# Performance work log

Hardware: AMD Instinct MI355X
Metric: run time of the kernel (lower is better)

The kernel has to match this reference:

```python
import jax, jax.numpy as jnp
import numpy as np

B, S, D, H = 2, 2048, 2048, 16
HD = D // H  # 128


def setup_inputs() -> dict:
    key = jax.random.key(0)
    ks = jax.random.split(key, 6)
    hidden_states = jax.random.normal(ks[0], (B, S, D), dtype=jnp.float32)
    # RoPE frequencies (llama-style): theta_j = 10000^(-2j/HD), angle = pos * theta
    inv_freq = 1.0 / (10000.0 ** (jnp.arange(0, HD, 2, dtype=jnp.float32) / HD))  # [HD/2]
    angles = jnp.arange(S, dtype=jnp.float32)[:, None] * inv_freq[None, :]  # [S, HD/2]
    freq_cos = jnp.cos(angles)
    freq_sin = jnp.sin(angles)
    # additive causal mask [1,1,S,S]
    neg = jnp.finfo(jnp.float32).min
    attention_mask = jnp.where(jnp.tril(jnp.ones((S, S), dtype=bool)), 0.0, neg)[None, None]
    std = 1.0 / np.sqrt(D)
    wq = jax.random.normal(ks[1], (D, D), dtype=jnp.float32) * std
    wk = jax.random.normal(ks[2], (D, D), dtype=jnp.float32) * std
    wv = jax.random.normal(ks[3], (D, D), dtype=jnp.float32) * std
    wo = jax.random.normal(ks[4], (D, D), dtype=jnp.float32) * std
    return dict(hidden_states=hidden_states, freq_cos=freq_cos, freq_sin=freq_sin,
                attention_mask=attention_mask, wq=wq, wk=wk, wv=wv, wo=wo)


def _apply_rope(x, cos, sin):
    # x: [B,S,H,HD]; cos/sin: [S,HD/2] broadcast to [1,S,1,HD/2]
    xr = x[..., ::2]
    xi = x[..., 1::2]
    c = cos[None, :, None, :]
    s = sin[None, :, None, :]
    or_ = xr * c - xi * s
    oi_ = xr * s + xi * c
    return jnp.stack((or_, oi_), axis=-1).reshape(x.shape)


def reference(hidden_states, freq_cos, freq_sin, attention_mask, wq, wk, wv, wo):
    bsz, q_len, _ = hidden_states.shape
    q = hidden_states @ wq.T
    k = hidden_states @ wk.T
    v = hidden_states @ wv.T
    q = q.reshape(bsz, q_len, H, HD)
    k = k.reshape(bsz, q_len, H, HD)
    v = v.reshape(bsz, q_len, H, HD)
    q = _apply_rope(q, freq_cos, freq_sin)
    k = _apply_rope(k, freq_cos, freq_sin)
    # [B,H,S,HD]
    q = q.transpose(0, 2, 1, 3)
    k = k.transpose(0, 2, 1, 3)
    v = v.transpose(0, 2, 1, 3)
    scores = jnp.einsum('bhqd,bhkd->bhqk', q, k) / jnp.sqrt(jnp.float32(HD))
    scores = scores + attention_mask
    attn = jax.nn.softmax(scores, axis=-1)
    out = jnp.einsum('bhqk,bhkd->bhqd', attn, v)
    out = out.transpose(0, 2, 1, 3).reshape(bsz, q_len, D)
    return out @ wo.T
```

## Files before the change

### kernel.cpp

```cpp
#include <hip/hip_runtime.h>

typedef unsigned short u16;
typedef unsigned int u32;
typedef __bf16 bf16x8 __attribute__((ext_vector_type(8)));
typedef float f32x4 __attribute__((ext_vector_type(4)));

#define B_ 2
#define S_ 2048
#define D_ 2048
#define H_ 16
#define HD_ 128

__device__ __forceinline__ u16 f2bf(float f) {
  u32 u = __float_as_uint(f);
  u32 r = (u + 0x7fffu + ((u >> 16) & 1u)) >> 16;
  return (u16)r;
}
__device__ __forceinline__ float bf2f(u16 b) {
  return __uint_as_float(((u32)b) << 16);
}

__device__ __forceinline__ void gll16(const void* g, void* lds) {
  __builtin_amdgcn_global_load_lds(
      (const __attribute__((address_space(1))) u32*)g,
      (__attribute__((address_space(3))) u32*)lds, 16, 0, 0);
}

__global__ __launch_bounds__(256) void cvt_bf16(const float* __restrict__ in,
                                                u16* __restrict__ out, int n4) {
  int i = blockIdx.x * 256 + threadIdx.x;
  if (i >= n4) return;
  float4 v = ((const float4*)in)[i];
  u16 o[4] __attribute__((aligned(8)));
  o[0] = f2bf(v.x); o[1] = f2bf(v.y); o[2] = f2bf(v.z); o[3] = f2bf(v.w);
  ((ushort4*)out)[i] = *(const ushort4*)o;
}

__global__ __launch_bounds__(256) void rope_k(u16* __restrict__ x,
                                              const float* __restrict__ cosb,
                                              const float* __restrict__ sinb,
                                              float scale) {
  int tid = blockIdx.x * 256 + threadIdx.x;
  int flat = tid << 3;
  int hd0 = flat & (HD_ - 1);
  int s = (flat >> 7) & (S_ - 1);
  u16 e[8] __attribute__((aligned(16)));
  *(uint4*)e = *(const uint4*)&x[flat];
  const float* cp = cosb + s * (HD_ / 2) + (hd0 >> 1);
  const float* sp = sinb + s * (HD_ / 2) + (hd0 >> 1);
#pragma unroll
  for (int i = 0; i < 4; ++i) {
    float xr = bf2f(e[2 * i]), xi = bf2f(e[2 * i + 1]);
    float c = cp[i], sn = sp[i];
    e[2 * i]     = f2bf((xr * c - xi * sn) * scale);
    e[2 * i + 1] = f2bf((xr * sn + xi * c) * scale);
  }
  *(uint4*)&x[flat] = *(const uint4*)e;
}

__global__ __launch_bounds__(256) void transpose_v(const u16* __restrict__ v,
                                                   u16* __restrict__ vt) {
  __shared__ u16 tile[64][72];
  int s0 = blockIdx.x * 64, hd0 = blockIdx.y * 64, bh = blockIdx.z;
  const u16* vh = v + (size_t)bh * S_ * HD_;
  u16* vth = vt + (size_t)bh * S_ * HD_;
  int t = threadIdx.x;
#pragma unroll
  for (int it = 0; it < 2; ++it) {
    int f = it * 256 + t;
    int r = f >> 3, c = (f & 7) * 8;
    *(uint4*)&tile[r][c] = *(const uint4*)&vh[(size_t)(s0 + r) * HD_ + hd0 + c];
  }
  __syncthreads();
#pragma unroll
  for (int it = 0; it < 2; ++it) {
    int f = it * 256 + t;
    int r = f >> 3, c = (f & 7) * 8;
    u16 tmp[8] __attribute__((aligned(16)));
#pragma unroll
    for (int j = 0; j < 8; ++j) tmp[j] = tile[c + j][r];
    *(uint4*)&vth[(size_t)(hd0 + r) * S_ + s0 + c] = *(const uint4*)tmp;
  }
}

__global__ __launch_bounds__(256) void gemm_bt(
    const u16* __restrict__ A,
    const u16* __restrict__ Wq, const u16* __restrict__ Wk, const u16* __restrict__ Wv,
    u16* __restrict__ Dq, u16* __restrict__ Dk, u16* __restrict__ Dv,
    float* __restrict__ DF, int outf32) {
  const u16* W = (blockIdx.z == 0) ? Wq : (blockIdx.z == 1) ? Wk : Wv;
  u16* Db = (blockIdx.z == 0) ? Dq : (blockIdx.z == 1) ? Dk : Dv;
  __shared__ u16 At[128 * 64] __attribute__((aligned(16)));
  __shared__ u16 Bt[128 * 64] __attribute__((aligned(16)));
  const int t = threadIdx.x, l = t & 63;
  const int w = t >> 6, wr = w >> 1, wc = w & 1;
  const int m0 = blockIdx.y * 128, n0 = blockIdx.x * 128;
  f32x4 acc[4][4];
#pragma unroll
  for (int i = 0; i < 4; ++i)
#pragma unroll
    for (int j = 0; j < 4; ++j) acc[i][j] = (f32x4){0.f, 0.f, 0.f, 0.f};
  const int row_s = t >> 3;
  const int col_s = (t & 7) * 8;
  for (int kt = 0; kt < 2048; kt += 64) {
    __syncthreads();
#pragma unroll
    for (int it = 0; it < 4; ++it) {
      int f = it * 256 + t;
      int row = it * 32 + row_s;
      gll16(&A[(size_t)(m0 + row) * 2048 + kt + col_s], &At[f * 8]);
      gll16(&W[(size_t)(n0 + row) * 2048 + kt + col_s], &Bt[f * 8]);
    }
    __syncthreads();
#pragma unroll
    for (int kk = 0; kk < 2; ++kk) {
      const int ko = kk * 32 + (l >> 4) * 8;
      bf16x8 av[4], bv[4];
#pragma unroll
      for (int i = 0; i < 4; ++i)
        av[i] = *(const bf16x8*)&At[(wr * 64 + i * 16 + (l & 15)) * 64 + ko];
#pragma unroll
      for (int i = 0; i < 4; ++i)
        bv[i] = *(const bf16x8*)&Bt[(wc * 64 + i * 16 + (l & 15)) * 64 + ko];
#pragma unroll
      for (int i = 0; i < 4; ++i)
#pragma unroll
        for (int j = 0; j < 4; ++j)
          acc[i][j] = __builtin_amdgcn_mfma_f32_16x16x32_bf16(av[i], bv[j], acc[i][j], 0, 0, 0);
    }
  }
#pragma unroll
  for (int i = 0; i < 4; ++i) {
#pragma unroll
    for (int j = 0; j < 4; ++j) {
#pragma unroll
      for (int r = 0; r < 4; ++r) {
        int m = m0 + wr * 64 + i * 16 + (l >> 4) * 4 + r;
        int n = n0 + wc * 64 + j * 16 + (l & 15);
        float val = acc[i][j][r];
        if (outf32) {
          DF[(size_t)m * 2048 + n] = val;
        } else {
          int b = m >> 11, s = m & 2047, h = n >> 7, hd = n & 127;
          Db[(((size_t)(b * 16 + h)) * 2048 + s) * 128 + hd] = f2bf(val);
        }
      }
    }
  }
}

__global__ __launch_bounds__(512) void attn_fwd(
    const u16* __restrict__ q, const u16* __restrict__ k, const u16* __restrict__ vt,
    u16* __restrict__ o) {
  const int fid = (int)blockIdx.x + 8 * (int)blockIdx.y;
  const int bh = fid & 31, xt = fid >> 5;
  const u16* qh = q + (size_t)bh * S_ * HD_;
  const u16* kh = k + (size_t)bh * S_ * HD_;
  const u16* vth = vt + (size_t)bh * S_ * HD_;
  const int t = threadIdx.x, l = t & 63, w = t >> 6;
  __shared__ u16 Kl[64][136] __attribute__((aligned(16)));
  __shared__ u16 Vl[128][72] __attribute__((aligned(16)));
  __shared__ u16 Pl[8][16][72] __attribute__((aligned(16)));
  const int b = bh >> 4, h = bh & 15;
  const int krr = t >> 4, krc = (t & 15) * 8;
  const int vrr = t >> 3, vrc = (t & 7) * 8;

  for (int half = 0; half < 2; ++half) {
    const int qb = half ? (15 - xt) : xt;
    const int q0 = qb * 128;
    const int wrow0 = q0 + w * 16;
    const int qrow = wrow0 + (l & 15);
    bf16x8 qf[4];
#pragma unroll
    for (int kk = 0; kk < 4; ++kk)
      qf[kk] = *(const bf16x8*)&qh[(size_t)qrow * HD_ + kk * 32 + (l >> 4) * 8];
    f32x4 oacc[8];
#pragma unroll
    for (int i = 0; i < 8; ++i) oacc[i] = (f32x4){0.f, 0.f, 0.f, 0.f};
    float mrow[4] = {-1e30f, -1e30f, -1e30f, -1e30f};
    float lrow[4] = {0.f, 0.f, 0.f, 0.f};

    const int ntile = 2 * qb + 2;
    for (int tk = 0; tk < ntile; ++tk) {
      const int kv0 = tk * 64;
      __syncthreads();
#pragma unroll
      for (int it = 0; it < 2; ++it) {
        int row = it * 32 + krr;
        *(uint4*)&Kl[row][krc] = *(const uint4*)&kh[(size_t)(kv0 + row) * HD_ + krc];
      }
#pragma unroll
      for (int it = 0; it < 2; ++it) {
        int row = it * 64 + vrr;
        *(uint4*)&Vl[row][vrc] = *(const uint4*)&vth[(size_t)row * S_ + kv0 + vrc];
      }
      __syncthreads();

      if (kv0 > wrow0 + 15) continue;

      f32x4 sf[4];
#pragma unroll
      for (int cb = 0; cb < 4; ++cb) sf[cb] = (f32x4){0.f, 0.f, 0.f, 0.f};
      __builtin_amdgcn_s_setprio(1);
#pragma unroll
      for (int kk = 0; kk < 4; ++kk) {
        const int ko = kk * 32 + (l >> 4) * 8;
#pragma unroll
        for (int cb = 0; cb < 4; ++cb) {
          bf16x8 bfr = *(const bf16x8*)&Kl[cb * 16 + (l & 15)][ko];
          sf[cb] = __builtin_amdgcn_mfma_f32_16x16x32_bf16(qf[kk], bfr, sf[cb], 0, 0, 0);
        }
      }
      __builtin_amdgcn_s_setprio(0);
      if (kv0 + 63 > wrow0) {
#pragma unroll
        for (int cb = 0; cb < 4; ++cb) {
          int c_abs = kv0 + cb * 16 + (l & 15);
#pragma unroll
          for (int r = 0; r < 4; ++r)
            if (c_abs > wrow0 + (l >> 4) * 4 + r) sf[cb][r] = -1e30f;
        }
      }
      float fr[4], ps[4];
#pragma unroll
      for (int r = 0; r < 4; ++r) {
        float v0 = fmaxf(fmaxf(sf[0][r], sf[1][r]), fmaxf(sf[2][r], sf[3][r]));
        v0 = fmaxf(v0, __shfl_xor(v0, 1));
        v0 = fmaxf(v0, __shfl_xor(v0, 2));
        v0 = fmaxf(v0, __shfl_xor(v0, 4));
        v0 = fmaxf(v0, __shfl_xor(v0, 8));
        float Mn = fmaxf(mrow[r], v0);
        fr[r] = exp2f(mrow[r] - Mn);
        mrow[r] = Mn;
        ps[r] = 0.f;
      }
#pragma unroll
      for (int cb = 0; cb < 4; ++cb) {
#pragma unroll
        for (int r = 0; r < 4; ++r) {
          float p = exp2f(sf[cb][r] - mrow[r]);
          ps[r] += p;
          Pl[w][(l >> 4) * 4 + r][cb * 16 + (l & 15)] = f2bf(p);
        }
      }
#pragma unroll
      for (int r = 0; r < 4; ++r) lrow[r] = lrow[r] * fr[r] + ps[r];
#pragma unroll
      for (int i = 0; i < 8; ++i)
#pragma unroll
        for (int r = 0; r < 4; ++r) oacc[i][r] *= fr[r];
      __builtin_amdgcn_s_setprio(1);
#pragma unroll
      for (int ks = 0; ks < 2; ++ks) {
        bf16x8 pa = *(const bf16x8*)&Pl[w][l & 15][ks * 32 + (l >> 4) * 8];
#pragma unroll
        for (int nf = 0; nf < 8; ++nf) {
          bf16x8 vb = *(const bf16x8*)&Vl[nf * 16 + (l & 15)][ks * 32 + (l >> 4) * 8];
          oacc[nf] = __builtin_amdgcn_mfma_f32_16x16x32_bf16(pa, vb, oacc[nf], 0, 0, 0);
        }
      }
      __builtin_amdgcn_s_setprio(0);
    }

    float inv[4];
#pragma unroll
    for (int r = 0; r < 4; ++r) {
      float s = lrow[r];
      s += __shfl_xor(s, 1);
      s += __shfl_xor(s, 2);
      s += __shfl_xor(s, 4);
      s += __shfl_xor(s, 8);
      inv[r] = 1.f / s;
    }
#pragma unroll
    for (int nf = 0; nf < 8; ++nf) {
#pragma unroll
      for (int r = 0; r < 4; ++r) {
        int row = wrow0 + (l >> 4) * 4 + r;
        int col = h * 128 + nf * 16 + (l & 15);
        o[((size_t)(b * 2048 + row)) * 2048 + col] = f2bf(oacc[nf][r] * inv[r]);
      }
    }
  }
}

extern "C" void kernel_launch(void* const* d_in, const int* in_sizes, int n_in,
                              void* d_out, int out_size, void* d_ws, size_t ws_size,
                              hipStream_t stream) {
  (void)in_sizes; (void)n_in; (void)out_size; (void)ws_size;
  const float* hs   = (const float*)d_in[0];
  const float* fcos = (const float*)d_in[1];
  const float* fsin = (const float*)d_in[2];
  const float* wq = (const float*)d_in[4];
  const float* wk = (const float*)d_in[5];
  const float* wv = (const float*)d_in[6];
  const float* wo = (const float*)d_in[7];
  float* out = (float*)d_out;
  char* ws = (char*)d_ws;
  u16* hsb = (u16*)(ws + 0);
  u16* wqb = (u16*)(ws + 16777216);
  u16* wkb = (u16*)(ws + 25165824);
  u16* wvb = (u16*)(ws + 33554432);
  u16* wob = (u16*)(ws + 41943040);
  u16* qb  = (u16*)(ws + 50331648);
  u16* kb  = (u16*)(ws + 67108864);
  u16* vb  = (u16*)(ws + 83886080);
  u16* vtb = (u16*)(ws + 100663296);
  u16* aob = (u16*)(ws + 117440512);

  cvt_bf16<<<8192, 256, 0, stream>>>(hs, hsb, 2097152);
  cvt_bf16<<<4096, 256, 0, stream>>>(wq, wqb, 1048576);
  cvt_bf16<<<4096, 256, 0, stream>>>(wk, wkb, 1048576);
  cvt_bf16<<<4096, 256, 0, stream>>>(wv, wvb, 1048576);
  cvt_bf16<<<4096, 256, 0, stream>>>(wo, wob, 1048576);

  gemm_bt<<<dim3(16, 32, 3), 256, 0, stream>>>(hsb, wqb, wkb, wvb, qb, kb, vb, nullptr, 0);

  const float qscale = (float)(0.08838834764831845 * 1.4426950408889634);
  rope_k<<<4096, 256, 0, stream>>>(qb, fcos, fsin, qscale);
  rope_k<<<4096, 256, 0, stream>>>(kb, fcos, fsin, 1.0f);

  transpose_v<<<dim3(32, 2, 32), 256, 0, stream>>>(vb, vtb);

  attn_fwd<<<dim3(8, 32), 512, 0, stream>>>(qb, kb, vtb, aob);

  gemm_bt<<<dim3(16, 32, 1), 256, 0, stream>>>(aob, wob, wob, wob,
                                               nullptr, nullptr, nullptr, out, 1);
}
```

Before: 467.0 us.

## Replace GEMM with 256x256 double-buffered swizzled-LDS pipelined kernel

Replaces the 128x128 single-buffered projection GEMM with a 256x256 tile kernel using 512 threads, 128 KB of dynamic LDS double-buffered, and an XOR-swizzled layout to avoid bank conflicts. Global-to-LDS prefetch of the next K tile is interleaved with MFMA phases, using explicit barriers, waitcnt and setprio. Blocks are remapped with an XCD-aware ordering for L2 locality. The large LDS footprint and accumulator register use limit occupancy, and the output GEMM launches only 128 workgroups, which may underfill the GPU.

```diff
diff --git a/kernel.cpp b/kernel.cpp
--- a/kernel.cpp
+++ b/kernel.cpp
@@ -83,66 +83,148 @@
   }
 }
 
-__global__ __launch_bounds__(256) void gemm_bt(
+#define SBAR()  { __builtin_amdgcn_sched_barrier(0); __builtin_amdgcn_s_barrier(); }
+#define LGKM0() { asm volatile("s_waitcnt lgkmcnt(0)" ::: "memory"); __builtin_amdgcn_sched_barrier(0); }
+#define VM0()   { asm volatile("s_waitcnt vmcnt(0)" ::: "memory"); __builtin_amdgcn_sched_barrier(0); }
+
+#define LOADQ(mh, nh, bi)                                                      \
+  {                                                                            \
+    const char* Ab = (const char*)(ldsA + (bi)*32768);                         \
+    const char* Bb = (const char*)(ldsB + (bi)*32768);                         \
+    _Pragma("unroll")                                                          \
+    for (int i = 0; i < 4; ++i) {                                              \
+      int row = wm * 128 + (mh)*64 + i * 16 + (l & 15);                        \
+      a_[i][0] = *(const bf16x8*)(Ab + row * 128 + ab0);                       \
+      a_[i][1] = *(const bf16x8*)(Ab + row * 128 + (ab0 ^ 64));                \
+    }                                                                          \
+    _Pragma("unroll")                                                          \
+    for (int j = 0; j < 2; ++j) {                                              \
+      int row = wn * 64 + (nh)*32 + j * 16 + (l & 15);                         \
+      b_[j][0] = *(const bf16x8*)(Bb + row * 128 + ab0);                       \
+      b_[j][1] = *(const bf16x8*)(Bb + row * 128 + (ab0 ^ 64));                \
+    }                                                                          \
+  }
+
+#define MFMAQ(mh, nh)                                                          \
+  _Pragma("unroll")                                                            \
+  for (int i = 0; i < 4; ++i)                                                  \
+    _Pragma("unroll")                                                          \
+    for (int j = 0; j < 2; ++j)                                                \
+      _Pragma("unroll")                                                        \
+      for (int kk = 0; kk < 2; ++kk)                                           \
+        acc[(mh)*4 + i][(nh)*2 + j] = __builtin_amdgcn_mfma_f32_16x16x32_bf16( \
+            a_[i][kk], b_[j][kk], acc[(mh)*4 + i][(nh)*2 + j], 0, 0, 0);
+
+#define PHASE(mh, nh, bi, STAGE, TAIL)                                         \
+  {                                                                            \
+    bf16x8 a_[4][2], b_[2][2];                                                 \
+    LOADQ(mh, nh, bi)                                                          \
+    STAGE                                                                      \
+    SBAR()                                                                     \
+    LGKM0()                                                                    \
+    __builtin_amdgcn_s_setprio(1);                                             \
+    MFMAQ(mh, nh)                                                              \
+    __builtin_amdgcn_s_setprio(0);                                             \
+    TAIL                                                                       \
+    SBAR()                                                                     \
+  }
+
+template <int MODE>
+__global__ __launch_bounds__(512, 2) void gemm256(
     const u16* __restrict__ A,
-    const u16* __restrict__ Wq, const u16* __restrict__ Wk, const u16* __restrict__ Wv,
+    const u16* __restrict__ W0, const u16* __restrict__ W1, const u16* __restrict__ W2,
     u16* __restrict__ Dq, u16* __restrict__ Dk, u16* __restrict__ Dv,
-    float* __restrict__ DF, int outf32) {
-  const u16* W = (blockIdx.z == 0) ? Wq : (blockIdx.z == 1) ? Wk : Wv;
-  u16* Db = (blockIdx.z == 0) ? Dq : (blockIdx.z == 1) ? Dk : Dv;
-  __shared__ u16 At[128 * 64] __attribute__((aligned(16)));
-  __shared__ u16 Bt[128 * 64] __attribute__((aligned(16)));
+    float* __restrict__ DF) {
+  extern __shared__ __align__(16) u16 lds[];
+  u16* ldsA = lds;
+  u16* ldsB = lds + 16384;
+  const int bx = (int)blockIdx.x;
+  const int nwg = (MODE == 0) ? 384 : 128;
+  const int cpx = nwg >> 3;
+  const int wg = (bx & 7) * cpx + (bx >> 3);
+  const int mt = wg & 15, nt = wg >> 4;
+  const int m0 = mt * 256;
+  const u16* W;
+  int n0w, wsel = 0;
+  if (MODE == 0) {
+    wsel = nt >> 3;
+    W = (wsel == 0) ? W0 : ((wsel == 1) ? W1 : W2);
+    n0w = (nt & 7) * 256;
+  } else {
+    W = W0;
+    n0w = nt * 256;
+  }
   const int t = threadIdx.x, l = t & 63;
-  const int w = t >> 6, wr = w >> 1, wc = w & 1;
-  const int m0 = blockIdx.y * 128, n0 = blockIdx.x * 128;
-  f32x4 acc[4][4];
-#pragma unroll
-  for (int i = 0; i < 4; ++i)
+  const int w = t >> 6, wm = w >> 2, wn = w & 3;
+  const int srow = t >> 3;
+  const int scol = (((t & 7) * 16) ^ ((srow & 7) << 4)) >> 1;
+  const u16* pAs = A + (size_t)(m0 + srow) * 2048 + scol;
+  const u16* pBs = W + (size_t)(n0w + srow) * 2048 + scol;
+  const int ab0 = ((l >> 4) * 16) ^ ((l & 7) << 4);
+
+  f32x4 acc[8][4];
+#pragma unroll
+  for (int i = 0; i < 8; ++i)
 #pragma unroll
     for (int j = 0; j < 4; ++j) acc[i][j] = (f32x4){0.f, 0.f, 0.f, 0.f};
-  const int row_s = t >> 3;
-  const int col_s = (t & 7) * 8;
-  for (int kt = 0; kt < 2048; kt += 64) {
-    __syncthreads();
-#pragma unroll
-    for (int it = 0; it < 4; ++it) {
-      int f = it * 256 + t;
-      int row = it * 32 + row_s;
-      gll16(&A[(size_t)(m0 + row) * 2048 + kt + col_s], &At[f * 8]);
-      gll16(&W[(size_t)(n0 + row) * 2048 + kt + col_s], &Bt[f * 8]);
+
+#pragma unroll
+  for (int s = 0; s < 4; ++s) {
+    gll16(pAs + s * 131072, ldsA + s * 4096 + t * 8);
+    gll16(pBs + s * 131072, ldsB + s * 4096 + t * 8);
+  }
+  VM0()
+  SBAR()
+
+#pragma unroll 2
+  for (int tt = 0; tt < 32; ++tt) {
+    const int bi = tt & 1;
+    const int dst = (bi ^ 1) * 32768;
+    const int ko = (tt + 1) << 6;
+    const bool pf = (tt < 31);
+    PHASE(0, 0, bi,
+      { if (pf) {
+          gll16(pAs + ko,           ldsA + dst + t * 8);
+          gll16(pAs + ko + 131072,  ldsA + dst + 4096 + t * 8);
+          gll16(pBs + ko,           ldsB + dst + t * 8);
+          gll16(pBs + ko + 131072,  ldsB + dst + 4096 + t * 8);
+      } }, {})
+    PHASE(0, 1, bi,
+      { if (pf) {
+          gll16(pAs + ko + 262144,  ldsA + dst + 8192 + t * 8);
+          gll16(pAs + ko + 393216,  ldsA + dst + 12288 + t * 8);
+          gll16(pBs + ko + 262144,  ldsB + dst + 8192 + t * 8);
+          gll16(pBs + ko + 393216,  ldsB + dst + 12288 + t * 8);
+      } }, {})
+    PHASE(1, 0, bi, {}, {})
+    PHASE(1, 1, bi, {}, { asm volatile("s_waitcnt vmcnt(0)" ::: "memory"); })
+  }
+
+  if (MODE == 0) {
+    u16* Db = (wsel == 0) ? Dq : ((wsel == 1) ? Dk : Dv);
+#pragma unroll
+    for (int fi = 0; fi < 8; ++fi) {
+#pragma unroll
+      for (int fj = 0; fj < 4; ++fj) {
+#pragma unroll
+        for (int r = 0; r < 4; ++r) {
+          int m = m0 + wm * 128 + fi * 16 + (l >> 4) * 4 + r;
+          int nn = n0w + wn * 64 + fj * 16 + (l & 15);
+          int b = m >> 11, s = m & 2047, h = nn >> 7, hd = nn & 127;
+          Db[(((size_t)(b * 16 + h)) * 2048 + s) * 128 + hd] = f2bf(acc[fi][fj][r]);
+        }
+      }
     }
-    __syncthreads();
-#pragma unroll
-    for (int kk = 0; kk < 2; ++kk) {
-      const int ko = kk * 32 + (l >> 4) * 8;
-      bf16x8 av[4], bv[4];
-#pragma unroll
-      for (int i = 0; i < 4; ++i)
-        av[i] = *(const bf16x8*)&At[(wr * 64 + i * 16 + (l & 15)) * 64 + ko];
-#pragma unroll
-      for (int i = 0; i < 4; ++i)
-        bv[i] = *(const bf16x8*)&Bt[(wc * 64 + i * 16 + (l & 15)) * 64 + ko];
-#pragma unroll
-      for (int i = 0; i < 4; ++i)
-#pragma unroll
-        for (int j = 0; j < 4; ++j)
-          acc[i][j] = __builtin_amdgcn_mfma_f32_16x16x32_bf16(av[i], bv[j], acc[i][j], 0, 0, 0);
-    }
-  }
-#pragma unroll
-  for (int i = 0; i < 4; ++i) {
-#pragma unroll
-    for (int j = 0; j < 4; ++j) {
-#pragma unroll
-      for (int r = 0; r < 4; ++r) {
-        int m = m0 + wr * 64 + i * 16 + (l >> 4) * 4 + r;
-        int n = n0 + wc * 64 + j * 16 + (l & 15);
-        float val = acc[i][j][r];
-        if (outf32) {
-          DF[(size_t)m * 2048 + n] = val;
-        } else {
-          int b = m >> 11, s = m & 2047, h = n >> 7, hd = n & 127;
-          Db[(((size_t)(b * 16 + h)) * 2048 + s) * 128 + hd] = f2bf(val);
+  } else {
+#pragma unroll
+    for (int fi = 0; fi < 8; ++fi) {
+#pragma unroll
+      for (int fj = 0; fj < 4; ++fj) {
+#pragma unroll
+        for (int r = 0; r < 4; ++r) {
+          int m = m0 + wm * 128 + fi * 16 + (l >> 4) * 4 + r;
+          int nn = n0w + wn * 64 + fj * 16 + (l & 15);
+          DF[(size_t)m * 2048 + nn] = acc[fi][fj][r];
         }
       }
     }
@@ -308,13 +390,18 @@
   u16* vtb = (u16*)(ws + 100663296);
   u16* aob = (u16*)(ws + 117440512);
 
+  hipFuncSetAttribute((const void*)gemm256<0>,
+                      hipFuncAttributeMaxDynamicSharedMemorySize, 131072);
+  hipFuncSetAttribute((const void*)gemm256<1>,
+                      hipFuncAttributeMaxDynamicSharedMemorySize, 131072);
+
   cvt_bf16<<<8192, 256, 0, stream>>>(hs, hsb, 2097152);
   cvt_bf16<<<4096, 256, 0, stream>>>(wq, wqb, 1048576);
   cvt_bf16<<<4096, 256, 0, stream>>>(wk, wkb, 1048576);
   cvt_bf16<<<4096, 256, 0, stream>>>(wv, wvb, 1048576);
   cvt_bf16<<<4096, 256, 0, stream>>>(wo, wob, 1048576);
 
-  gemm_bt<<<dim3(16, 32, 3), 256, 0, stream>>>(hsb, wqb, wkb, wvb, qb, kb, vb, nullptr, 0);
+  gemm256<0><<<384, 512, 131072, stream>>>(hsb, wqb, wkb, wvb, qb, kb, vb, nullptr);
 
   const float qscale = (float)(0.08838834764831845 * 1.4426950408889634);
   rope_k<<<4096, 256, 0, stream>>>(qb, fcos, fsin, qscale);
@@ -324,6 +411,6 @@
 
   attn_fwd<<<dim3(8, 32), 512, 0, stream>>>(qb, kb, vtb, aob);
 
-  gemm_bt<<<dim3(16, 32, 1), 256, 0, stream>>>(aob, wob, wob, wob,
-                                               nullptr, nullptr, nullptr, out, 1);
-}
+  gemm256<1><<<128, 512, 131072, stream>>>(aob, wob, nullptr, nullptr,
+                                           nullptr, nullptr, nullptr, out);
+}
```

Result: no change. 463.7 us (-0.7%).

## Rewrite projection GEMMs with triple-buffered swizzled LDS pipeline and larger tiles

Applied to the files above, without the earlier changes.

Replaces the simple synchronous 128x128 GEMM with a 128x256-tile, 512-thread kernel that triple-buffers 64-wide K slices in dynamic LDS. Global-to-LDS loads are prefetched two stages ahead, tracked with explicit vmcnt waits, and read through an XOR swizzle to avoid bank conflicts. The kernel also raises MFMA priority and remaps workgroups for L2 locality. This is meant to hide load latency and cut barrier stalls in the QKV and output projections. In exchange it uses 144KB of LDS per block and relies on hand-tuned waitcnt ordering.

```diff
diff --git a/kernel.cpp b/kernel.cpp
--- a/kernel.cpp
+++ b/kernel.cpp
@@ -83,66 +83,130 @@
   }
 }
 
-__global__ __launch_bounds__(256) void gemm_bt(
+#define SBAR()  { __builtin_amdgcn_sched_barrier(0); __builtin_amdgcn_s_barrier(); }
+#define LGKM0() { asm volatile("s_waitcnt lgkmcnt(0)" ::: "memory"); __builtin_amdgcn_sched_barrier(0); }
+#define VMC6()  { asm volatile("s_waitcnt vmcnt(6)" ::: "memory"); __builtin_amdgcn_sched_barrier(0); }
+#define VMC0()  { asm volatile("s_waitcnt vmcnt(0)" ::: "memory"); __builtin_amdgcn_sched_barrier(0); }
+
+#define GPHASE(Ab, Bb, COL, PRE, TAILVM)                                        \
+  {                                                                             \
+    PRE                                                                         \
+    bf16x8 a_[4], b_[4];                                                        \
+    _Pragma("unroll") for (int i = 0; i < 4; ++i)                               \
+      a_[i] = *(const bf16x8*)((Ab) + (wm * 64 + i * 16 + (l & 15)) * 128 + (COL)); \
+    _Pragma("unroll") for (int j = 0; j < 4; ++j)                               \
+      b_[j] = *(const bf16x8*)((Bb) + (wn * 64 + j * 16 + (l & 15)) * 128 + (COL)); \
+    SBAR(); LGKM0();                                                            \
+    __builtin_amdgcn_s_setprio(1);                                              \
+    _Pragma("unroll") for (int i = 0; i < 4; ++i)                               \
+      _Pragma("unroll") for (int j = 0; j < 4; ++j)                             \
+        acc[i][j] = __builtin_amdgcn_mfma_f32_16x16x32_bf16(a_[i], b_[j], acc[i][j], 0, 0, 0); \
+    __builtin_amdgcn_s_setprio(0);                                              \
+    TAILVM                                                                      \
+    SBAR();                                                                     \
+  }
+
+#define GTILE(cur, kpf, PF, TAILVM)                                             \
+  {                                                                             \
+    char* Ab = lds + (cur) * 49152;                                             \
+    char* Bb = Ab + 16384;                                                      \
+    GPHASE(Ab, Bb, ab0,                                                         \
+      { if (PF) {                                                               \
+          char* An = lds + (((cur) + 2) % 3) * 49152;                           \
+          char* Bn = An + 16384;                                                \
+          gll16(pAs + (kpf), An + t * 16);                                      \
+          gll16(pAs + (kpf) + 131072, An + 8192 + t * 16);                      \
+          gll16(pBs + (kpf), Bn + t * 16);                                      \
+          gll16(pBs + (kpf) + 131072, Bn + 8192 + t * 16);                      \
+          gll16(pBs + (kpf) + 262144, Bn + 16384 + t * 16);                     \
+          gll16(pBs + (kpf) + 393216, Bn + 24576 + t * 16);                     \
+      } }, {})                                                                  \
+    GPHASE(Ab, Bb, ab1, {}, TAILVM)                                             \
+  }
+
+template <int MODE>
+__global__ __launch_bounds__(512, 2) void gemm128(
     const u16* __restrict__ A,
-    const u16* __restrict__ Wq, const u16* __restrict__ Wk, const u16* __restrict__ Wv,
+    const u16* __restrict__ W0, const u16* __restrict__ W1, const u16* __restrict__ W2,
     u16* __restrict__ Dq, u16* __restrict__ Dk, u16* __restrict__ Dv,
-    float* __restrict__ DF, int outf32) {
-  const u16* W = (blockIdx.z == 0) ? Wq : (blockIdx.z == 1) ? Wk : Wv;
-  u16* Db = (blockIdx.z == 0) ? Dq : (blockIdx.z == 1) ? Dk : Dv;
-  __shared__ u16 At[128 * 64] __attribute__((aligned(16)));
-  __shared__ u16 Bt[128 * 64] __attribute__((aligned(16)));
+    float* __restrict__ DF) {
+  extern __shared__ __align__(16) char lds[];
+  const int bx = (int)blockIdx.x;
+  const int nwg = (MODE == 0) ? 768 : 256;
+  const int cpx = nwg >> 3;
+  const int wg = (bx & 7) * cpx + (bx >> 3);
+  const int mt = wg & 31, nt = wg >> 5;
+  const int m0 = mt * 128;
+  const u16* W;
+  int n0w, wsel = 0;
+  if (MODE == 0) {
+    int ng = nt * 256;
+    wsel = ng >> 11;
+    W = (wsel == 0) ? W0 : ((wsel == 1) ? W1 : W2);
+    n0w = ng & 2047;
+  } else {
+    W = W0;
+    n0w = nt * 256;
+  }
   const int t = threadIdx.x, l = t & 63;
-  const int w = t >> 6, wr = w >> 1, wc = w & 1;
-  const int m0 = blockIdx.y * 128, n0 = blockIdx.x * 128;
+  const int w = t >> 6, wm = w >> 2, wn = w & 3;
+  const int srow = t >> 3;
+  const int scol = ((((t & 7) * 16) ^ ((srow & 7) << 4)) >> 1);
+  const u16* pAs = A + (size_t)(m0 + srow) * 2048 + scol;
+  const u16* pBs = W + (size_t)(n0w + srow) * 2048 + scol;
+  const int ab0 = ((l >> 4) * 16) ^ ((l & 7) << 4);
+  const int ab1 = ab0 ^ 64;
+
   f32x4 acc[4][4];
 #pragma unroll
   for (int i = 0; i < 4; ++i)
 #pragma unroll
     for (int j = 0; j < 4; ++j) acc[i][j] = (f32x4){0.f, 0.f, 0.f, 0.f};
-  const int row_s = t >> 3;
-  const int col_s = (t & 7) * 8;
-  for (int kt = 0; kt < 2048; kt += 64) {
-    __syncthreads();
-#pragma unroll
-    for (int it = 0; it < 4; ++it) {
-      int f = it * 256 + t;
-      int row = it * 32 + row_s;
-      gll16(&A[(size_t)(m0 + row) * 2048 + kt + col_s], &At[f * 8]);
-      gll16(&W[(size_t)(n0 + row) * 2048 + kt + col_s], &Bt[f * 8]);
-    }
-    __syncthreads();
-#pragma unroll
-    for (int kk = 0; kk < 2; ++kk) {
-      const int ko = kk * 32 + (l >> 4) * 8;
-      bf16x8 av[4], bv[4];
-#pragma unroll
-      for (int i = 0; i < 4; ++i)
-        av[i] = *(const bf16x8*)&At[(wr * 64 + i * 16 + (l & 15)) * 64 + ko];
-#pragma unroll
-      for (int i = 0; i < 4; ++i)
-        bv[i] = *(const bf16x8*)&Bt[(wc * 64 + i * 16 + (l & 15)) * 64 + ko];
-#pragma unroll
-      for (int i = 0; i < 4; ++i)
-#pragma unroll
-        for (int j = 0; j < 4; ++j)
-          acc[i][j] = __builtin_amdgcn_mfma_f32_16x16x32_bf16(av[i], bv[j], acc[i][j], 0, 0, 0);
-    }
-  }
-#pragma unroll
-  for (int i = 0; i < 4; ++i) {
-#pragma unroll
-    for (int j = 0; j < 4; ++j) {
-#pragma unroll
-      for (int r = 0; r < 4; ++r) {
-        int m = m0 + wr * 64 + i * 16 + (l >> 4) * 4 + r;
-        int n = n0 + wc * 64 + j * 16 + (l & 15);
-        float val = acc[i][j][r];
-        if (outf32) {
-          DF[(size_t)m * 2048 + n] = val;
-        } else {
-          int b = m >> 11, s = m & 2047, h = n >> 7, hd = n & 127;
-          Db[(((size_t)(b * 16 + h)) * 2048 + s) * 128 + hd] = f2bf(val);
+
+#pragma unroll
+  for (int s = 0; s < 2; ++s) gll16(pAs + s * 131072, lds + s * 8192 + t * 16);
+#pragma unroll
+  for (int s = 0; s < 4; ++s) gll16(pBs + s * 131072, lds + 16384 + s * 8192 + t * 16);
+#pragma unroll
+  for (int s = 0; s < 2; ++s) gll16(pAs + 64 + s * 131072, lds + 49152 + s * 8192 + t * 16);
+#pragma unroll
+  for (int s = 0; s < 4; ++s) gll16(pBs + 64 + s * 131072, lds + 49152 + 16384 + s * 8192 + t * 16);
+  VMC6()
+  SBAR()
+
+  for (int tb = 0; tb < 10; ++tb) {
+    GTILE(0, (tb * 3 + 2) * 64, 1, VMC6())
+    GTILE(1, (tb * 3 + 3) * 64, 1, VMC6())
+    GTILE(2, (tb * 3 + 4) * 64, 1, VMC6())
+  }
+  GTILE(0, 0, 0, VMC0())
+  GTILE(1, 0, 0, {})
+
+  if (MODE == 0) {
+    u16* Db = (wsel == 0) ? Dq : ((wsel == 1) ? Dk : Dv);
+#pragma unroll
+    for (int fi = 0; fi < 4; ++fi) {
+#pragma unroll
+      for (int fj = 0; fj < 4; ++fj) {
+#pragma unroll
+        for (int r = 0; r < 4; ++r) {
+          int m = m0 + wm * 64 + fi * 16 + (l >> 4) * 4 + r;
+          int nn = n0w + wn * 64 + fj * 16 + (l & 15);
+          int b = m >> 11, s = m & 2047, h = nn >> 7, hd = nn & 127;
+          Db[(((size_t)(b * 16 + h)) * 2048 + s) * 128 + hd] = f2bf(acc[fi][fj][r]);
+        }
+      }
+    }
+  } else {
+#pragma unroll
+    for (int fi = 0; fi < 4; ++fi) {
+#pragma unroll
+      for (int fj = 0; fj < 4; ++fj) {
+#pragma unroll
+        for (int r = 0; r < 4; ++r) {
+          int m = m0 + wm * 64 + fi * 16 + (l >> 4) * 4 + r;
+          int nn = n0w + wn * 64 + fj * 16 + (l & 15);
+          DF[(size_t)m * 2048 + nn] = acc[fi][fj][r];
         }
       }
     }
@@ -308,13 +372,18 @@
   u16* vtb = (u16*)(ws + 100663296);
   u16* aob = (u16*)(ws + 117440512);
 
+  hipFuncSetAttribute((const void*)gemm128<0>,
+                      hipFuncAttributeMaxDynamicSharedMemorySize, 147456);
+  hipFuncSetAttribute((const void*)gemm128<1>,
+                      hipFuncAttributeMaxDynamicSharedMemorySize, 147456);
+
   cvt_bf16<<<8192, 256, 0, stream>>>(hs, hsb, 2097152);
   cvt_bf16<<<4096, 256, 0, stream>>>(wq, wqb, 1048576);
   cvt_bf16<<<4096, 256, 0, stream>>>(wk, wkb, 1048576);
   cvt_bf16<<<4096, 256, 0, stream>>>(wv, wvb, 1048576);
   cvt_bf16<<<4096, 256, 0, stream>>>(wo, wob, 1048576);
 
-  gemm_bt<<<dim3(16, 32, 3), 256, 0, stream>>>(hsb, wqb, wkb, wvb, qb, kb, vb, nullptr, 0);
+  gemm128<0><<<768, 512, 147456, stream>>>(hsb, wqb, wkb, wvb, qb, kb, vb, nullptr);
 
   const float qscale = (float)(0.08838834764831845 * 1.4426950408889634);
   rope_k<<<4096, 256, 0, stream>>>(qb, fcos, fsin, qscale);
@@ -324,6 +393,6 @@
 
   attn_fwd<<<dim3(8, 32), 512, 0, stream>>>(qb, kb, vtb, aob);
 
-  gemm_bt<<<dim3(16, 32, 1), 256, 0, stream>>>(aob, wob, wob, wob,
-                                               nullptr, nullptr, nullptr, out, 1);
-}
+  gemm128<1><<<256, 512, 147456, stream>>>(aob, wob, nullptr, nullptr,
+                                           nullptr, nullptr, nullptr, out);
+}
```

Result: faster. 419.3 us (-10.2%).
